# Optimization experiments

Hardware: AMD Instinct MI355X
Metric: run time of the kernel (lower is better)

Reference implementation:

```python
import jax, jax.numpy as jnp
import numpy as np

C = 64
D = C // 8  # query/key channels
B, H, W = 4, 64, 64


def setup_inputs() -> dict:
    key = jax.random.key(0)
    ks = jax.random.split(key, 8)
    x = jax.random.normal(ks[0], (B, C, H, W), dtype=jnp.float32)
    # 1x1 conv params (kernel squeezed to [out_ch, in_ch])
    sq = 1.0 / np.sqrt(C)
    Wq = jax.random.uniform(ks[1], (D, C), jnp.float32, -sq, sq)
    bq = jax.random.uniform(ks[2], (D,), jnp.float32, -sq, sq)
    Wk = jax.random.uniform(ks[3], (D, C), jnp.float32, -sq, sq)
    bk = jax.random.uniform(ks[4], (D,), jnp.float32, -sq, sq)
    Wv = jax.random.uniform(ks[5], (C, C), jnp.float32, -sq, sq)
    bv = jax.random.uniform(ks[6], (C,), jnp.float32, -sq, sq)
    # gamma is zero-initialized in the module; use a nonzero value so the
    # attention path actually contributes to the output.
    gamma = jax.random.normal(ks[7], (1,), dtype=jnp.float32)
    return {"x": x, "Wq": Wq, "bq": bq, "Wk": Wk, "bk": bk, "Wv": Wv, "bv": bv, "gamma": gamma}


def reference(x, Wq, bq, Wk, bk, Wv, bv, gamma):
    b, c, h, w = x.shape
    n = h * w
    xf = x.reshape(b, c, n)                                   # [B,C,N]
    q = jnp.einsum('dc,bcn->bdn', Wq, xf) + bq[None, :, None]  # [B,D,N]
    k = jnp.einsum('dc,bcn->bdn', Wk, xf) + bk[None, :, None]  # [B,D,N]
    v = jnp.einsum('ec,bcn->ben', Wv, xf) + bv[None, :, None]  # [B,C,N]
    energy = jnp.einsum('bdn,bdm->bnm', q, k)                  # [B,N,N] = Q^T K
    attn = jax.nn.softmax(energy, axis=-1)                     # softmax over keys m
    # out[b,c,n] = sum_m v[b,c,m] * attn[b,n,m]  (V @ attention^T in torch)
    out = jnp.einsum('bcm,bnm->bcn', v, attn).reshape(b, c, h, w)
    return gamma[0] * out + x
```

## Files before the change

kernel.cpp:

```cpp
#include <hip/hip_runtime.h>
#include <hip/hip_bf16.h>
#include <math.h>

#define BB 4
#define CC 64
#define DD 8
#define NN 4096
#define KS 4
#define KPS (NN / KS)
#define VSTR 516
#define KSTR 12
#define LOG2E 1.44269504088896340736f

typedef __attribute__((ext_vector_type(4))) short short4v;
typedef __attribute__((ext_vector_type(8))) short short8s;
typedef __attribute__((ext_vector_type(4))) unsigned short ushort4v;
typedef __attribute__((ext_vector_type(8))) unsigned short ushort8;
typedef __attribute__((ext_vector_type(16))) float f32x16;

#if defined(__HIP_DEVICE_COMPILE__)
  #if __has_builtin(__builtin_amdgcn_mfma_f32_32x32x8bf16_1k)
    #define MFMA32x8(A, B, C) __builtin_amdgcn_mfma_f32_32x32x8bf16_1k(A, B, C, 0, 0, 0)
  #elif __has_builtin(__builtin_amdgcn_mfma_f32_32x32x8_bf16)
    #define MFMA32x8(A, B, C) __builtin_amdgcn_mfma_f32_32x32x8_bf16(A, B, C, 0, 0, 0)
  #else
    #error "no 32x32x8 bf16 MFMA builtin in device pass"
  #endif
  #if __has_builtin(__builtin_amdgcn_exp2f)
    #define EXP2(x) __builtin_amdgcn_exp2f(x)
  #else
    #define EXP2(x) exp2f(x)
  #endif
#else
  static __device__ __host__ inline f32x16 MFMA32x8(short4v, short4v, f32x16 c) { return c; }
  #define EXP2(x) exp2f(x)
#endif

static __device__ inline f32x16 PVMFMA(short8s A, short8s B, f32x16 c) {
#if defined(__HIP_DEVICE_COMPILE__) && __has_builtin(__builtin_amdgcn_mfma_f32_32x32x16_bf16)
    typedef __attribute__((ext_vector_type(8))) __bf16 bf16x8;
    return __builtin_amdgcn_mfma_f32_32x32x16_bf16(
        __builtin_bit_cast(bf16x8, A), __builtin_bit_cast(bf16x8, B), c, 0, 0, 0);
#else
    union { short8s v; short4v h[2]; } a, b;
    a.v = A; b.v = B;
    return MFMA32x8(a.h[1], b.h[1], MFMA32x8(a.h[0], b.h[0], c));
#endif
}

static __device__ inline short4v pack4(float a, float b, float c, float d) {
    union { short4v s; __hip_bfloat162 h[2]; } u;
    u.h[0] = __float22bfloat162_rn(make_float2(a, b));
    u.h[1] = __float22bfloat162_rn(make_float2(c, d));
    return u.s;
}
static __device__ inline unsigned packu(float lo, float hi) {
    union { __hip_bfloat162 h; unsigned u; } t;
    t.h = __float22bfloat162_rn(make_float2(lo, hi));
    return t.u;
}

__global__ __launch_bounds__(64) void qkv_kernel(
    const float* __restrict__ x,  const float* __restrict__ Wq, const float* __restrict__ bq,
    const float* __restrict__ Wk, const float* __restrict__ bk,
    const float* __restrict__ Wv, const float* __restrict__ bv,
    unsigned short* __restrict__ qb, unsigned short* __restrict__ kb,
    unsigned short* __restrict__ vT)
{
    __shared__ unsigned short LQ[32 * 8];
    __shared__ unsigned short LK[32 * 8];

    int lane = threadIdx.x & 63;
    int l32 = lane & 31, h2 = lane >> 5;

    int blk = blockIdx.x;
    int b = blk & (BB - 1);
    int ng = blk >> 2;
    int n0 = ng * 32;

    const float* xb = x + (size_t)b * CC * NN + n0 + l32;
    short4v bf[8];
    #pragma unroll
    for (int s = 0; s < 8; ++s) {
        int c0 = s * 8 + 4 * h2;
        float x0 = xb[(size_t)(c0 + 0) * NN];
        float x1 = xb[(size_t)(c0 + 1) * NN];
        float x2 = xb[(size_t)(c0 + 2) * NN];
        float x3 = xb[(size_t)(c0 + 3) * NN];
        bf[s] = pack4(x0, x1, x2, x3);
    }

    #pragma unroll
    for (int rt = 0; rt < 2; ++rt) {
        short4v af[8];
        #pragma unroll
        for (int s = 0; s < 8; ++s) {
            float4 w4 = *(const float4*)(Wv + (size_t)(rt * 32 + l32) * CC + s * 8 + 4 * h2);
            af[s] = pack4(w4.x, w4.y, w4.z, w4.w);
        }
        f32x16 acc;
        #pragma unroll
        for (int r = 0; r < 16; ++r) acc[r] = 0.f;
        #pragma unroll
        for (int s = 0; s < 8; ++s)
            acc = MFMA32x8(af[s], bf[s], acc);
        #pragma unroll
        for (int r = 0; r < 16; ++r) {
            int row = rt * 32 + (r & 3) + 8 * (r >> 2) + 4 * h2;
            float val = acc[r] + bv[row];
            __hip_bfloat16 hv = __float2bfloat16(val);
            vT[((size_t)b * CC + row) * NN + n0 + l32] = *(unsigned short*)&hv;
        }
    }

    {
        short4v af[8];
        #pragma unroll
        for (int s = 0; s < 8; ++s) {
            float4 w4;
            if (l32 < 8) {
                w4 = *(const float4*)(Wq + (size_t)l32 * CC + s * 8 + 4 * h2);
            } else if (l32 < 16) {
                w4 = *(const float4*)(Wk + (size_t)(l32 - 8) * CC + s * 8 + 4 * h2);
            } else {
                w4 = make_float4(0.f, 0.f, 0.f, 0.f);
            }
            af[s] = pack4(w4.x, w4.y, w4.z, w4.w);
        }
        f32x16 acc;
        #pragma unroll
        for (int r = 0; r < 16; ++r) acc[r] = 0.f;
        #pragma unroll
        for (int s = 0; s < 8; ++s)
            acc = MFMA32x8(af[s], bf[s], acc);

        short4v qp = pack4((acc[0] + bq[0 + 4 * h2]) * LOG2E,
                           (acc[1] + bq[1 + 4 * h2]) * LOG2E,
                           (acc[2] + bq[2 + 4 * h2]) * LOG2E,
                           (acc[3] + bq[3 + 4 * h2]) * LOG2E);
        short4v kp = pack4(acc[4] + bk[0 + 4 * h2],
                           acc[5] + bk[1 + 4 * h2],
                           acc[6] + bk[2 + 4 * h2],
                           acc[7] + bk[3 + 4 * h2]);
        *(short4v*)(LQ + (size_t)l32 * 8 + 4 * h2) = qp;
        *(short4v*)(LK + (size_t)l32 * 8 + 4 * h2) = kp;
        __syncthreads();
        int rw = lane & 31;
        if (lane < 32) {
            ushort8 row = *(const ushort8*)(LQ + (size_t)rw * 8);
            *(ushort8*)(qb + ((size_t)b * NN + n0 + rw) * 8) = row;
        } else {
            ushort8 row = *(const ushort8*)(LK + (size_t)rw * 8);
            *(ushort8*)(kb + ((size_t)b * NN + n0 + rw) * 8) = row;
        }
    }
}

__global__ __launch_bounds__(512, 2) void flash_kernel(
    const unsigned short* __restrict__ qb, const unsigned short* __restrict__ kb,
    const unsigned short* __restrict__ vT, unsigned* __restrict__ accb,
    float* __restrict__ sbuf)
{
    __shared__ unsigned short VS[2][64 * VSTR];
    __shared__ unsigned short KL[2][512 * KSTR];
    int tid = threadIdx.x;
    int wave = tid >> 6, lane = tid & 63;
    int l32 = lane & 31, h2 = lane >> 5;

    int blk = blockIdx.x;
    int b = blk & (BB - 1);
    int qchunk = (blk >> 2) & 15;
    int split = blk >> 6;
    int n0 = qchunk * 256 + wave * 32;

    short4v qf = *(const short4v*)(qb + ((size_t)b * NN + n0 + l32) * DD + h2 * 4);

    const unsigned short* kbb = kb + (size_t)b * NN * DD;
    const unsigned short* vbb = vT + (size_t)b * CC * NN;
    int m0 = split * KPS;

    int ch = tid >> 3, s8 = (tid & 7) * 8;
    const unsigned short* vg = vbb + (size_t)ch * NN + m0 + s8;

    {
        ushort8 v[8];
        #pragma unroll
        for (int k = 0; k < 8; ++k) v[k] = *(const ushort8*)(vg + 64 * k);
        ushort8 kA = *(const ushort8*)(kbb + (size_t)(m0 + tid) * DD);

        unsigned short* vp = VS[0] + (size_t)ch * VSTR + s8;
        #pragma unroll
        for (int k = 0; k < 8; ++k) {
            *(ushort4v*)(vp + 64 * k)     = *(ushort4v*)&v[k];
            *(ushort4v*)(vp + 64 * k + 4) = *((ushort4v*)&v[k] + 1);
        }
        unsigned short* p = KL[0] + (size_t)tid * KSTR;
        *(ushort4v*)(p)     = *(ushort4v*)&kA;
        *(ushort4v*)(p + 4) = *((ushort4v*)&kA + 1);
    }
    __syncthreads();

    ushort8 v1[8];
    #pragma unroll
    for (int k = 0; k < 8; ++k) v1[k] = *(const ushort8*)(vg + 512 + 64 * k);
    ushort8 kA1 = *(const ushort8*)(kbb + (size_t)(m0 + 512 + tid) * DD);

    union { short8s v; unsigned short e[8]; } ones;
    #pragma unroll
    for (int i = 0; i < 8; ++i) ones.e[i] = 0x3F80;

    f32x16 o0, o1, oS, zz;
    #pragma unroll
    for (int r = 0; r < 16; ++r) { o0[r] = 0.f; o1[r] = 0.f; oS[r] = 0.f; zz[r] = 0.f; }

#define COMPUTE(ST)                                                              \
    {                                                                            \
        _Pragma("unroll")                                                        \
        for (int s = 0; s < 16; ++s) {                                           \
            short4v kf = *(const short4v*)(KL[ST] + (size_t)(s * 32 + l32) * KSTR + h2 * 4); \
            f32x16 sv = MFMA32x8(kf, qf, zz);                                    \
            float w[16];                                                         \
            _Pragma("unroll")                                                    \
            for (int r = 0; r < 16; ++r) w[r] = EXP2(sv[r]);                     \
            union { short4v s; __hip_bfloat162 h[2]; } u[4];                     \
            _Pragma("unroll")                                                    \
            for (int g = 0; g < 4; ++g) {                                        \
                u[g].h[0] = __float22bfloat162_rn(make_float2(w[4 * g],     w[4 * g + 1])); \
                u[g].h[1] = __float22bfloat162_rn(make_float2(w[4 * g + 2], w[4 * g + 3])); \
            }                                                                    \
            _Pragma("unroll")                                                    \
            for (int j = 0; j < 2; ++j) {                                        \
                int kb0 = s * 32 + j * 16 + h2 * 4;                              \
                union { short8s v; short4v h[2]; } A, B0, B1;                    \
                A.h[0] = u[2 * j].s;                                             \
                A.h[1] = u[2 * j + 1].s;                                         \
                B0.h[0] = *(const short4v*)(VS[ST] + (size_t)(l32)      * VSTR + kb0);     \
                B0.h[1] = *(const short4v*)(VS[ST] + (size_t)(l32)      * VSTR + kb0 + 8); \
                B1.h[0] = *(const short4v*)(VS[ST] + (size_t)(32 + l32) * VSTR + kb0);     \
                B1.h[1] = *(const short4v*)(VS[ST] + (size_t)(32 + l32) * VSTR + kb0 + 8); \
                o0 = PVMFMA(A.v, B0.v, o0);                                      \
                o1 = PVMFMA(A.v, B1.v, o1);                                      \
                oS = PVMFMA(A.v, ones.v, oS);                                    \
            }                                                                    \
        }                                                                        \
    }

    COMPUTE(0)

    {
        unsigned short* vp = VS[1] + (size_t)ch * VSTR + s8;
        #pragma unroll
        for (int k = 0; k < 8; ++k) {
            *(ushort4v*)(vp + 64 * k)     = *(ushort4v*)&v1[k];
            *(ushort4v*)(vp + 64 * k + 4) = *((ushort4v*)&v1[k] + 1);
        }
        unsigned short* p = KL[1] + (size_t)tid * KSTR;
        *(ushort4v*)(p)     = *(ushort4v*)&kA1;
        *(ushort4v*)(p + 4) = *((ushort4v*)&kA1 + 1);
    }
    __syncthreads();

    COMPUTE(1)
#undef COMPUTE

    unsigned* au = accb + (((size_t)((b * KS + split) * 128 + qchunk * 8 + wave)) << 10);
    #pragma unroll
    for (int r = 0; r < 16; ++r)
        au[r * 64 + lane] = packu(o0[r], o1[r]);

    float* sb = sbuf + (size_t)(b * KS + split) * NN + n0;
    #pragma unroll
    for (int r = 0; r < 16; ++r) {
        int ql = (r & 3) + 8 * (r >> 2) + 4 * h2;
        if (l32 == r) sb[ql] = oS[r];
    }
}

__global__ __launch_bounds__(256) void norm_kernel(
    const unsigned* __restrict__ accb, const float* __restrict__ sbuf,
    const float* __restrict__ x, const float* __restrict__ gamma,
    float* __restrict__ out)
{
    __shared__ float tile[16 * 65];
    __shared__ float stl[16];
    int blk = blockIdx.x;
    int t = blk & 7;
    int uu = blk >> 3;
    int b = t & 3;
    int qpar = t >> 2;
    int qhalf = uu & 1;
    int sub = (uu >> 1) & 7;
    int qhi = uu >> 4;
    int qchunk = qhi * 2 + qpar;
    int g32 = qchunk * 8 + sub;
    int n0 = g32 * 32 + qhalf * 16;
    int tid = threadIdx.x;

    if (tid < 16) {
        float st = 0.f;
        #pragma unroll
        for (int sp = 0; sp < KS; ++sp)
            st += sbuf[(size_t)(b * KS + sp) * NN + n0 + tid];
        stl[tid] = 1.0f / st;
    }

    int spoff = tid >> 7;
    int u = tid & 127;
    int rl = u >> 4;
    int lane0 = (u & 15) * 4;

    float alo[4], ahi[4];
    #pragma unroll
    for (int e = 0; e < 4; ++e) { alo[e] = 0.f; ahi[e] = 0.f; }
    #pragma unroll
    for (int p = 0; p < KS / 2; ++p) {
        int sp = p * 2 + spoff;
        const unsigned* base = accb + (((size_t)((b * KS + sp) * 128 + g32)) << 10)
                             + qhalf * 512;
        uint4 v = *(const uint4*)(base + u * 4);
        unsigned wv[4] = {v.x, v.y, v.z, v.w};
        #pragma unroll
        for (int e = 0; e < 4; ++e) {
            alo[e] += __uint_as_float(wv[e] << 16);
            ahi[e] += __uint_as_float(wv[e] & 0xFFFF0000u);
        }
    }

    #pragma unroll
    for (int e = 0; e < 4; ++e) {
        int lane = lane0 + e;
        int h2 = lane >> 5, l32 = lane & 31;
        int ql = (rl & 3) + 8 * ((rl >> 2) & 1) + 4 * h2;
        if (tid < 128) {
            tile[ql * 65 + l32]      = alo[e];
            tile[ql * 65 + 32 + l32] = ahi[e];
        }
    }
    __syncthreads();
    #pragma unroll
    for (int e = 0; e < 4; ++e) {
        int lane = lane0 + e;
        int h2 = lane >> 5, l32 = lane & 31;
        int ql = (rl & 3) + 8 * ((rl >> 2) & 1) + 4 * h2;
        if (tid >= 128) {
            tile[ql * 65 + l32]      += alo[e];
            tile[ql * 65 + 32 + l32] += ahi[e];
        }
    }
    __syncthreads();

    float gm = gamma[0];
    #pragma unroll
    for (int p2 = 0; p2 < 4; ++p2) {
        int idx = p2 * 256 + tid;
        int c = idx >> 4, ql = idx & 15;
        size_t xi = ((size_t)b * CC + c) * NN + n0 + ql;
        out[xi] = gm * tile[ql * 65 + c] * stl[ql] + x[xi];
    }
}

extern "C" void kernel_launch(void* const* d_in, const int* in_sizes, int n_in,
                              void* d_out, int out_size, void* d_ws, size_t ws_size,
                              hipStream_t stream)
{
    const float* x     = (const float*)d_in[0];
    const float* Wq    = (const float*)d_in[1];
    const float* bq    = (const float*)d_in[2];
    const float* Wk    = (const float*)d_in[3];
    const float* bk    = (const float*)d_in[4];
    const float* Wv    = (const float*)d_in[5];
    const float* bv    = (const float*)d_in[6];
    const float* gamma = (const float*)d_in[7];
    float* out = (float*)d_out;

    float* ws = (float*)d_ws;
    size_t off = 0;
    unsigned short* qb = (unsigned short*)(ws + off); off += (size_t)BB * NN * DD / 2 + 64;
    unsigned short* kb = (unsigned short*)(ws + off); off += (size_t)BB * NN * DD / 2 + 64;
    unsigned short* vT = (unsigned short*)(ws + off); off += (size_t)BB * CC * NN / 2 + 64;
    unsigned* accb = (unsigned*)(ws + off); off += (size_t)BB * KS * NN * CC / 2;
    float* sbuf = ws + off; off += (size_t)BB * KS * NN;

    qkv_kernel<<<BB * 128, 64, 0, stream>>>(x, Wq, bq, Wk, bk, Wv, bv, qb, kb, vT);
    flash_kernel<<<KS * 16 * BB, 512, 0, stream>>>(qb, kb, vT, accb, sbuf);
    norm_kernel<<<BB * 256, 256, 0, stream>>>(accb, sbuf, x, gamma, out);
}
```

Baseline: 93.79 us.

## Fuse split-K normalization into flash kernel via last-block atomic counter

Removes the separate norm kernel. Each flash block increments a per-(batch, query-chunk) atomic counter after writing its partial accumulators, and the last of the KS split blocks reduces all splits, normalizes and writes the output. This saves one kernel launch and the gap between kernels, but the reduction now runs on only 64 blocks, in a serialized tail, instead of 1024 small blocks. It also adds a memset and thread fences.

```diff
diff --git a/kernel.cpp b/kernel.cpp
--- a/kernel.cpp
+++ b/kernel.cpp
@@ -159,10 +159,14 @@
 __global__ __launch_bounds__(512, 2) void flash_kernel(
     const unsigned short* __restrict__ qb, const unsigned short* __restrict__ kb,
     const unsigned short* __restrict__ vT, unsigned* __restrict__ accb,
-    float* __restrict__ sbuf)
+    float* __restrict__ sbuf, int* __restrict__ cnt,
+    const float* __restrict__ x, const float* __restrict__ gamma,
+    float* __restrict__ out)
 {
     __shared__ unsigned short VS[2][64 * VSTR];
     __shared__ unsigned short KL[2][512 * KSTR];
+    __shared__ float stl[256];
+    __shared__ int isLast;
     int tid = threadIdx.x;
     int wave = tid >> 6, lane = tid & 63;
     int l32 = lane & 31, h2 = lane >> 5;
@@ -274,88 +278,65 @@
         int ql = (r & 3) + 8 * (r >> 2) + 4 * h2;
         if (l32 == r) sb[ql] = oS[r];
     }
-}
-
-__global__ __launch_bounds__(256) void norm_kernel(
-    const unsigned* __restrict__ accb, const float* __restrict__ sbuf,
-    const float* __restrict__ x, const float* __restrict__ gamma,
-    float* __restrict__ out)
-{
-    __shared__ float tile[16 * 65];
-    __shared__ float stl[16];
-    int blk = blockIdx.x;
-    int t = blk & 7;
-    int uu = blk >> 3;
-    int b = t & 3;
-    int qpar = t >> 2;
-    int qhalf = uu & 1;
-    int sub = (uu >> 1) & 7;
-    int qhi = uu >> 4;
-    int qchunk = qhi * 2 + qpar;
-    int g32 = qchunk * 8 + sub;
-    int n0 = g32 * 32 + qhalf * 16;
-    int tid = threadIdx.x;
-
-    if (tid < 16) {
+
+    __threadfence();
+    __syncthreads();
+    if (tid == 0) {
+        int gid = b * 16 + qchunk;
+        int old = atomicAdd(&cnt[gid], 1);
+        isLast = (old == KS - 1);
+    }
+    __syncthreads();
+    if (!isLast) return;
+    __threadfence();
+
+    float* tile = (float*)VS;
+    if (tid < 256) {
         float st = 0.f;
         #pragma unroll
         for (int sp = 0; sp < KS; ++sp)
-            st += sbuf[(size_t)(b * KS + sp) * NN + n0 + tid];
+            st += sbuf[(size_t)(b * KS + sp) * NN + qchunk * 256 + tid];
         stl[tid] = 1.0f / st;
     }
 
-    int spoff = tid >> 7;
-    int u = tid & 127;
-    int rl = u >> 4;
-    int lane0 = (u & 15) * 4;
-
-    float alo[4], ahi[4];
-    #pragma unroll
-    for (int e = 0; e < 4; ++e) { alo[e] = 0.f; ahi[e] = 0.f; }
-    #pragma unroll
-    for (int p = 0; p < KS / 2; ++p) {
-        int sp = p * 2 + spoff;
-        const unsigned* base = accb + (((size_t)((b * KS + sp) * 128 + g32)) << 10)
-                             + qhalf * 512;
-        uint4 v = *(const uint4*)(base + u * 4);
-        unsigned wv[4] = {v.x, v.y, v.z, v.w};
+    size_t gb0 = ((size_t)(b * KS) * 128 + qchunk * 8) << 10;
+    const size_t spstride = (size_t)128 << 10;
+    #pragma unroll
+    for (int it = 0; it < 4; ++it) {
+        int off4 = it * 512 + tid;
+        const unsigned* p0 = accb + gb0 + (size_t)off4 * 4;
+        float alo[4] = {0.f, 0.f, 0.f, 0.f}, ahi[4] = {0.f, 0.f, 0.f, 0.f};
+        #pragma unroll
+        for (int sp = 0; sp < KS; ++sp) {
+            uint4 v = *(const uint4*)(p0 + (size_t)sp * spstride);
+            unsigned wv[4] = {v.x, v.y, v.z, v.w};
+            #pragma unroll
+            for (int e = 0; e < 4; ++e) {
+                alo[e] += __uint_as_float(wv[e] << 16);
+                ahi[e] += __uint_as_float(wv[e] & 0xFFFF0000u);
+            }
+        }
+        int w   = off4 >> 8;
+        int r   = (off4 >> 4) & 15;
+        int h2r = (off4 & 15) >> 3;
+        int l3b = (off4 & 7) * 4;
+        int ql  = w * 32 + (r & 3) + 8 * (r >> 2) + 4 * h2r;
         #pragma unroll
         for (int e = 0; e < 4; ++e) {
-            alo[e] += __uint_as_float(wv[e] << 16);
-            ahi[e] += __uint_as_float(wv[e] & 0xFFFF0000u);
-        }
-    }
-
-    #pragma unroll
-    for (int e = 0; e < 4; ++e) {
-        int lane = lane0 + e;
-        int h2 = lane >> 5, l32 = lane & 31;
-        int ql = (rl & 3) + 8 * ((rl >> 2) & 1) + 4 * h2;
-        if (tid < 128) {
-            tile[ql * 65 + l32]      = alo[e];
-            tile[ql * 65 + 32 + l32] = ahi[e];
-        }
-    }
-    __syncthreads();
-    #pragma unroll
-    for (int e = 0; e < 4; ++e) {
-        int lane = lane0 + e;
-        int h2 = lane >> 5, l32 = lane & 31;
-        int ql = (rl & 3) + 8 * ((rl >> 2) & 1) + 4 * h2;
-        if (tid >= 128) {
-            tile[ql * 65 + l32]      += alo[e];
-            tile[ql * 65 + 32 + l32] += ahi[e];
+            tile[ql * 65 + l3b + e]      = alo[e];
+            tile[ql * 65 + 32 + l3b + e] = ahi[e];
         }
     }
     __syncthreads();
 
     float gm = gamma[0];
     #pragma unroll
-    for (int p2 = 0; p2 < 4; ++p2) {
-        int idx = p2 * 256 + tid;
-        int c = idx >> 4, ql = idx & 15;
-        size_t xi = ((size_t)b * CC + c) * NN + n0 + ql;
-        out[xi] = gm * tile[ql * 65 + c] * stl[ql] + x[xi];
+    for (int p = 0; p < 32; ++p) {
+        int idx = p * 512 + tid;
+        int c   = idx >> 8;
+        int nq  = idx & 255;
+        size_t xi = ((size_t)b * CC + c) * NN + qchunk * 256 + nq;
+        out[xi] = gm * tile[nq * 65 + c] * stl[nq] + x[xi];
     }
 }
 
@@ -380,8 +361,10 @@
     unsigned short* vT = (unsigned short*)(ws + off); off += (size_t)BB * CC * NN / 2 + 64;
     unsigned* accb = (unsigned*)(ws + off); off += (size_t)BB * KS * NN * CC / 2;
     float* sbuf = ws + off; off += (size_t)BB * KS * NN;
-
+    int* cnt = (int*)(ws + off); off += 64;
+
+    hipMemsetAsync(cnt, 0, 64 * sizeof(int), stream);
     qkv_kernel<<<BB * 128, 64, 0, stream>>>(x, Wq, bq, Wk, bk, Wv, bv, qb, kb, vT);
-    flash_kernel<<<KS * 16 * BB, 512, 0, stream>>>(qb, kb, vT, accb, sbuf);
-    norm_kernel<<<BB * 256, 256, 0, stream>>>(accb, sbuf, x, gamma, out);
-}
+    flash_kernel<<<KS * 16 * BB, 512, 0, stream>>>(qb, kb, vT, accb, sbuf, cnt,
+                                                   x, gamma, out);
+}
```

Result: slower. 145.4 us (+55.1%).
